# Performance work log

Measured on AMD Instinct MI355X. Metric: run time of the kernel, lower is better.

## Reference

```python
import jax, jax.numpy as jnp
import numpy as np

B, T, D = 4, 2048, 1024
F = 4 * D  # Config.RWKV_INTERMIDATE_SIZE * hidden_dim
LN_EPS = 1e-3  # keras LayerNormalization default epsilon


def layer_norm(x, g, b, eps=LN_EPS):
    mu = jnp.mean(x, axis=-1, keepdims=True)
    var = jnp.mean(jnp.square(x - mu), axis=-1, keepdims=True)
    return (x - mu) * jax.lax.rsqrt(var + eps) * g + b


def setup_inputs() -> dict:
    ks = jax.random.split(jax.random.key(0), 24)
    g = lambda k, shape: (jax.random.normal(k, shape, jnp.float32)
                          * np.sqrt(2.0 / sum(shape)))  # ~glorot
    return {
        "x": jax.random.normal(ks[0], (B, T, D), jnp.float32),
        "s_cm": jnp.zeros((B, D), jnp.float32),
        "s_tm": jnp.zeros((B, D), jnp.float32),
        "s_num": jnp.zeros((B, D), jnp.float32),
        "s_den": jnp.zeros((B, D), jnp.float32),
        "s_q": jnp.zeros((B, D), jnp.float32),
        "ln1_g": jnp.ones((D,), jnp.float32),
        "ln1_b": jnp.zeros((D,), jnp.float32),
        "ln2_g": jnp.ones((D,), jnp.float32),
        "ln2_b": jnp.zeros((D,), jnp.float32),
        "tm_mix_k": jax.random.uniform(ks[1], (D,), jnp.float32, 0.0, 2.0 / D),
        "tm_mix_v": jax.random.uniform(ks[2], (D,), jnp.float32, 0.0, 2.0 / D),
        "tm_mix_r": jax.random.uniform(ks[3], (D,), jnp.float32, 0.0, (2.0 / D) ** 0.5),
        "tm_kw": g(ks[4], (D, D)),
        "tm_vw": g(ks[5], (D, D)),
        "tm_rw": g(ks[6], (D, D)),
        "time_decay": jax.random.uniform(ks[7], (D,), jnp.float32, 0.0, 0.1),
        "time_first": jax.random.uniform(ks[8], (D,), jnp.float32, 0.0, 0.05),
        "out_w": g(ks[9], (D, D)),
        "cm_mix_k": jax.random.uniform(ks[10], (D,), jnp.float32, 0.0, 2.0 / D),
        "cm_mix_r": jax.random.uniform(ks[11], (D,), jnp.float32, 0.0, 2.0 / D),
        "cm_kw": g(ks[12], (D, F)),
        "cm_vw": g(ks[13], (F, D)),
        "cm_rw": g(ks[14], (D, D)),
    }


def _shift(h, s):
    # token shift: prepend last-token state, drop last timestep
    return jnp.concatenate([s[:, None, :], h[:, :-1, :]], axis=1)


def reference(x, s_cm, s_tm, s_num, s_den, s_q,
              ln1_g, ln1_b, ln2_g, ln2_b,
              tm_mix_k, tm_mix_v, tm_mix_r, tm_kw, tm_vw, tm_rw,
              time_decay, time_first, out_w,
              cm_mix_k, cm_mix_r, cm_kw, cm_vw, cm_rw):
    # ---- time mixing ----
    h = layer_norm(x, ln1_g, ln1_b)  # [B,T,D]
    hs = _shift(h, s_tm)
    xk = h * tm_mix_k + hs * (1.0 - tm_mix_k)
    xv = h * tm_mix_v + hs * (1.0 - tm_mix_v)
    xr = h * tm_mix_r + hs * (1.0 - tm_mix_r)
    k = xk @ tm_kw  # [B,T,D]
    v = xv @ tm_vw
    r = jax.nn.sigmoid(xr @ tm_rw)
    w = -jnp.exp(time_decay)  # [D]

    def step(carry, kv):
        num, den, q = carry
        kt, vt = kv  # [B,D]
        mo = jnp.maximum(q, kt + time_first)
        e1 = jnp.exp(q - mo)
        e2 = jnp.exp(kt + time_first - mo)
        out = (e1 * num + e2 * vt) / (e1 * den + e2)
        ms = jnp.maximum(q + w, kt)
        e1s = jnp.exp(q + w - ms)
        e2s = jnp.exp(kt - ms)
        return (e1s * num + e2s * vt, e1s * den + e2s, ms), out

    (num, den, q), wkv = jax.lax.scan(
        step, (s_num, s_den, s_q),
        (k.transpose(1, 0, 2), v.transpose(1, 0, 2)))
    wkv = wkv.transpose(1, 0, 2)  # [B,T,D]
    x = x + (r * wkv) @ out_w

    # ---- channel mixing ----
    h2 = layer_norm(x, ln2_g, ln2_b)
    hs2 = _shift(h2, s_cm)
    xk2 = h2 * cm_mix_k + hs2 * (1.0 - cm_mix_k)
    xr2 = h2 * cm_mix_r + hs2 * (1.0 - cm_mix_r)
    kv = jnp.square(jax.nn.relu(xk2 @ cm_kw)) @ cm_vw  # [B,T,F] -> [B,T,D]
    x = x + jax.nn.sigmoid(xr2 @ cm_rw) * kv

    # new state: (cm_inputs, tm_inputs, num, den, q)
    return x, h2[:, -1], h[:, -1], num, den, q
```

## Files before the change

### kernel.cpp

```cpp
#include <hip/hip_runtime.h>

typedef unsigned short ushort_t;
typedef __attribute__((ext_vector_type(8))) short short8;
typedef __attribute__((ext_vector_type(4))) float f32x4;

#define B_ 4
#define T_ 2048
#define D_ 1024
#define F_ 4096
#define M_ (B_*T_)
#define CH_ 64
#define NC_ (T_/CH_)

#define AS1 __attribute__((address_space(1)))
#define AS3 __attribute__((address_space(3)))

__device__ __forceinline__ ushort_t f2bf(float f) {
  union { float f; unsigned u; } a; a.f = f;
  unsigned r = a.u + 0x7FFFu + ((a.u >> 16) & 1u);
  return (ushort_t)(r >> 16);
}

__device__ __forceinline__ void gl_lds16(const void* g, void* l) {
  __builtin_amdgcn_global_load_lds((AS1 void*)(__UINTPTR_TYPE__)g,
                                   (AS3 void*)l, 16, 0, 0);
}

__global__ __launch_bounds__(256) void tconv(const float* __restrict__ W,
                                             ushort_t* __restrict__ Wt,
                                             int K, int N) {
  __shared__ float tile[32][33];
  int tx = threadIdx.x, ty = threadIdx.y;
  int n0 = blockIdx.x * 32, k0 = blockIdx.y * 32;
  #pragma unroll
  for (int i = 0; i < 32; i += 8)
    tile[ty + i][tx] = W[(size_t)(k0 + ty + i) * N + n0 + tx];
  __syncthreads();
  #pragma unroll
  for (int i = 0; i < 32; i += 8)
    Wt[(size_t)(n0 + ty + i) * K + k0 + tx] = f2bf(tile[tx][ty + i]);
}

__global__ __launch_bounds__(256) void ln_fwd(const float* __restrict__ x,
                                              const float* __restrict__ g,
                                              const float* __restrict__ bb,
                                              float* __restrict__ h,
                                              float* __restrict__ last) {
  int row = blockIdx.x;
  int tid = threadIdx.x;
  float4 v = ((const float4*)(x + (size_t)row * D_))[tid];
  float s1 = v.x + v.y + v.z + v.w;
  float s2 = v.x * v.x + v.y * v.y + v.z * v.z + v.w * v.w;
  #pragma unroll
  for (int o = 32; o > 0; o >>= 1) { s1 += __shfl_down(s1, o); s2 += __shfl_down(s2, o); }
  __shared__ float r1[4], r2[4];
  if ((tid & 63) == 0) { r1[tid >> 6] = s1; r2[tid >> 6] = s2; }
  __syncthreads();
  s1 = r1[0] + r1[1] + r1[2] + r1[3];
  s2 = r2[0] + r2[1] + r2[2] + r2[3];
  float mu = s1 * (1.0f / D_);
  float rs = rsqrtf(s2 * (1.0f / D_) - mu * mu + 1e-3f);
  float4 gv = ((const float4*)g)[tid];
  float4 bv = ((const float4*)bb)[tid];
  float4 o4;
  o4.x = (v.x - mu) * rs * gv.x + bv.x;
  o4.y = (v.y - mu) * rs * gv.y + bv.y;
  o4.z = (v.z - mu) * rs * gv.z + bv.z;
  o4.w = (v.w - mu) * rs * gv.w + bv.w;
  ((float4*)(h + (size_t)row * D_))[tid] = o4;
  if ((row & (T_ - 1)) == T_ - 1)
    ((float4*)(last + (size_t)(row >> 11) * D_))[tid] = o4;
}

#define MIX1(c, p, f) f2bf((c) * (f) + (p) * (1.0f - (f)))

__global__ __launch_bounds__(256) void mix_tm(const float* __restrict__ h,
                                              const float* __restrict__ st,
                                              const float* __restrict__ mk,
                                              const float* __restrict__ mv,
                                              const float* __restrict__ mr,
                                              ushort_t* __restrict__ xk,
                                              ushort_t* __restrict__ xv,
                                              ushort_t* __restrict__ xr) {
  size_t qi = (size_t)blockIdx.x * 256 + threadIdx.x;
  int dq = (int)(qi & 255);
  size_t td = qi >> 8;
  int t = (int)(td & (T_ - 1));
  int b = (int)(td >> 11);
  float4 hc = ((const float4*)h)[qi];
  float4 hp = (t == 0) ? ((const float4*)st)[b * 256 + dq] : ((const float4*)h)[qi - 256];
  float4 k4 = ((const float4*)mk)[dq];
  float4 v4 = ((const float4*)mv)[dq];
  float4 r4 = ((const float4*)mr)[dq];
  ushort4 ok, ov, orr;
  ok.x = MIX1(hc.x, hp.x, k4.x); ok.y = MIX1(hc.y, hp.y, k4.y);
  ok.z = MIX1(hc.z, hp.z, k4.z); ok.w = MIX1(hc.w, hp.w, k4.w);
  ov.x = MIX1(hc.x, hp.x, v4.x); ov.y = MIX1(hc.y, hp.y, v4.y);
  ov.z = MIX1(hc.z, hp.z, v4.z); ov.w = MIX1(hc.w, hp.w, v4.w);
  orr.x = MIX1(hc.x, hp.x, r4.x); orr.y = MIX1(hc.y, hp.y, r4.y);
  orr.z = MIX1(hc.z, hp.z, r4.z); orr.w = MIX1(hc.w, hp.w, r4.w);
  ((ushort4*)xk)[qi] = ok;
  ((ushort4*)xv)[qi] = ov;
  ((ushort4*)xr)[qi] = orr;
}

__global__ __launch_bounds__(256) void mix_cm(const float* __restrict__ h,
                                              const float* __restrict__ st,
                                              const float* __restrict__ mk,
                                              const float* __restrict__ mr,
                                              ushort_t* __restrict__ xk,
                                              ushort_t* __restrict__ xr) {
  size_t qi = (size_t)blockIdx.x * 256 + threadIdx.x;
  int dq = (int)(qi & 255);
  size_t td = qi >> 8;
  int t = (int)(td & (T_ - 1));
  int b = (int)(td >> 11);
  float4 hc = ((const float4*)h)[qi];
  float4 hp = (t == 0) ? ((const float4*)st)[b * 256 + dq] : ((const float4*)h)[qi - 256];
  float4 k4 = ((const float4*)mk)[dq];
  float4 r4 = ((const float4*)mr)[dq];
  ushort4 ok, orr;
  ok.x = MIX1(hc.x, hp.x, k4.x); ok.y = MIX1(hc.y, hp.y, k4.y);
  ok.z = MIX1(hc.z, hp.z, k4.z); ok.w = MIX1(hc.w, hp.w, k4.w);
  orr.x = MIX1(hc.x, hp.x, r4.x); orr.y = MIX1(hc.y, hp.y, r4.y);
  orr.z = MIX1(hc.z, hp.z, r4.z); orr.w = MIX1(hc.w, hp.w, r4.w);
  ((ushort4*)xk)[qi] = ok;
  ((ushort4*)xr)[qi] = orr;
}

__global__ __launch_bounds__(256) void wkv_part1(const float* __restrict__ k,
                                                 const float* __restrict__ v,
                                                 const float* __restrict__ tdec,
                                                 float* __restrict__ cn,
                                                 float* __restrict__ cd,
                                                 float* __restrict__ cq) {
  int idx = blockIdx.x * 256 + threadIdx.x;
  int d = idx & (D_ - 1);
  int b = (idx >> 10) & (B_ - 1);
  int c = idx >> 12;
  float w = -__expf(tdec[d]);
  const float* kp = k + ((size_t)b * T_ + c * CH_) * D_ + d;
  const float* vp = v + ((size_t)b * T_ + c * CH_) * D_ + d;
  float num = 0.0f, den = 0.0f, q = -1e30f;
  for (int t0 = 0; t0 < CH_; t0 += 8) {
    float kt[8], vt[8];
    #pragma unroll
    for (int i = 0; i < 8; ++i) {
      size_t off = (size_t)(t0 + i) * D_;
      kt[i] = kp[off]; vt[i] = vp[off];
    }
    #pragma unroll
    for (int i = 0; i < 8; ++i) {
      float kk = kt[i];
      float ms = fmaxf(q + w, kk);
      float e1 = __expf(q + w - ms), e2 = __expf(kk - ms);
      num = e1 * num + e2 * vt[i];
      den = e1 * den + e2;
      q = ms;
    }
  }
  cn[idx] = num; cd[idx] = den; cq[idx] = q;
}

__global__ __launch_bounds__(256) void wkv_part2(const float* __restrict__ cn,
                                                 const float* __restrict__ cd,
                                                 const float* __restrict__ cq,
                                                 const float* __restrict__ sn,
                                                 const float* __restrict__ sd,
                                                 const float* __restrict__ sq,
                                                 const float* __restrict__ tdec,
                                                 float* __restrict__ pn,
                                                 float* __restrict__ pd,
                                                 float* __restrict__ pq,
                                                 float* __restrict__ on,
                                                 float* __restrict__ od,
                                                 float* __restrict__ oq) {
  int idx = blockIdx.x * 256 + threadIdx.x;
  int d = idx & (D_ - 1);
  float w = -__expf(tdec[d]);
  float wL = w * (float)CH_;
  float num = sn[idx], den = sd[idx], q = sq[idx];
  #pragma unroll 4
  for (int c = 0; c < NC_; ++c) {
    int j = (c << 12) + idx;
    pn[j] = num; pd[j] = den; pq[j] = q;
    float m2 = cq[j];
    float qn = fmaxf(q + wL, m2);
    float e1 = __expf(q + wL - qn), e2 = __expf(m2 - qn);
    num = e1 * num + e2 * cn[j];
    den = e1 * den + e2 * cd[j];
    q = qn;
  }
  on[idx] = num; od[idx] = den; oq[idx] = q;
}

__global__ __launch_bounds__(256) void wkv_part3(const float* __restrict__ k,
                                                 const float* __restrict__ v,
                                                 const float* __restrict__ r,
                                                 const float* __restrict__ pn,
                                                 const float* __restrict__ pd,
                                                 const float* __restrict__ pq,
                                                 const float* __restrict__ tdec,
                                                 const float* __restrict__ tfirst,
                                                 ushort_t* __restrict__ rwkv) {
  int idx = blockIdx.x * 256 + threadIdx.x;
  int d = idx & (D_ - 1);
  int b = (idx >> 10) & (B_ - 1);
  int c = idx >> 12;
  float w = -__expf(tdec[d]);
  float tf = tfirst[d];
  float num = pn[idx], den = pd[idx], q = pq[idx];
  size_t base = ((size_t)b * T_ + c * CH_) * D_ + d;
  const float* kp = k + base;
  const float* vp = v + base;
  const float* rp = r + base;
  ushort_t* op = rwkv + base;
  for (int t0 = 0; t0 < CH_; t0 += 8) {
    float kt[8], vt[8], rt[8];
    #pragma unroll
    for (int i = 0; i < 8; ++i) {
      size_t off = (size_t)(t0 + i) * D_;
      kt[i] = kp[off]; vt[i] = vp[off]; rt[i] = rp[off];
    }
    #pragma unroll
    for (int i = 0; i < 8; ++i) {
      float kk = kt[i];
      float mo = fmaxf(q, kk + tf);
      float e1 = __expf(q - mo), e2 = __expf(kk + tf - mo);
      float o = (e1 * num + e2 * vt[i]) / (e1 * den + e2);
      op[(size_t)(t0 + i) * D_] = f2bf(rt[i] * o);
      float ms = fmaxf(q + w, kk);
      float e1s = __expf(q + w - ms), e2s = __expf(kk - ms);
      num = e1s * num + e2s * vt[i];
      den = e1s * den + e2s;
      q = ms;
    }
  }
}

template <int EPI>
__global__ __launch_bounds__(256)
void gemm128(const ushort_t* __restrict__ A, const ushort_t* __restrict__ Bt,
             int N, int K,
             float* __restrict__ Cf, ushort_t* __restrict__ Cb,
             const float* __restrict__ X, const float* __restrict__ X2,
             const float* __restrict__ Xb) {
  __shared__ alignas(16) ushort_t sA[128 * 64];
  __shared__ alignas(16) ushort_t sB[128 * 64];
  const int tid = threadIdx.x;
  const int m0 = blockIdx.x * 128, n0 = blockIdx.y * 128;
  const int lane = tid & 63, wave = tid >> 6;
  const int wm = (wave >> 1) * 64, wn = (wave & 1) * 64;
  const int lr = lane & 15;
  const int lk = (lane >> 4) * 8;

  const ushort_t* ga = A + (size_t)(m0 + (tid >> 3)) * K + (tid & 7) * 8;
  const ushort_t* gb = Bt + (size_t)(n0 + (tid >> 3)) * K + (tid & 7) * 8;
  ushort_t* la = sA + tid * 8;
  ushort_t* lb = sB + tid * 8;

  f32x4 acc[4][4] = {};

  const int ksteps = K >> 6;
  for (int kt = 0; kt < ksteps; ++kt) {
    const int kof = kt * 64;
    #pragma unroll
    for (int i = 0; i < 4; ++i) {
      gl_lds16(ga + (size_t)(i * 32) * K + kof, la + i * 2048);
      gl_lds16(gb + (size_t)(i * 32) * K + kof, lb + i * 2048);
    }
    __syncthreads();
    short8 af[2][4], bfr[2][4];
    #pragma unroll
    for (int s = 0; s < 2; ++s)
      #pragma unroll
      for (int i = 0; i < 4; ++i) {
        af[s][i]  = *(const short8*)&sA[(wm + i * 16 + lr) * 64 + s * 32 + lk];
        bfr[s][i] = *(const short8*)&sB[(wn + i * 16 + lr) * 64 + s * 32 + lk];
      }
    #pragma unroll
    for (int s = 0; s < 2; ++s)
      #pragma unroll
      for (int mi = 0; mi < 4; ++mi)
        #pragma unroll
        for (int ni = 0; ni < 4; ++ni)
          acc[mi][ni] = __builtin_amdgcn_mfma_f32_16x16x32_bf16(
              af[s][mi], bfr[s][ni], acc[mi][ni], 0, 0, 0);
    __syncthreads();
  }

  #pragma unroll
  for (int mi = 0; mi < 4; ++mi)
    #pragma unroll
    for (int ni = 0; ni < 4; ++ni)
      #pragma unroll
      for (int j = 0; j < 4; ++j) {
        int row = m0 + wm + mi * 16 + ((lane >> 4) << 2) + j;
        int col = n0 + wn + ni * 16 + lr;
        size_t idx = (size_t)row * N + col;
        float v = acc[mi][ni][j];
        if (EPI == 0) {
          Cf[idx] = v;
        } else if (EPI == 1) {
          Cf[idx] = 1.0f / (1.0f + __expf(-v));
        } else if (EPI == 2) {
          Cf[idx] = X[idx] + v;
        } else if (EPI == 4) {
          float s = 1.0f / (1.0f + __expf(-v));
          Cf[idx] = X2[idx] + s * (X[idx] + Xb[idx]);
        }
      }
}

template <int EPI>
__global__ __launch_bounds__(512, 2)
void gemm256(const ushort_t* __restrict__ A, const ushort_t* __restrict__ Bt,
             int N, int K, int ktn,
             float* __restrict__ Cf, float* __restrict__ Cf2,
             ushort_t* __restrict__ Cb) {
  __shared__ alignas(16) ushort_t sA[2][256 * 64];
  __shared__ alignas(16) ushort_t sB[2][256 * 64];
  const int tid = threadIdx.x;
  const int lane = tid & 63;
  const int wave = tid >> 6;
  const int wr = wave >> 2, wc = wave & 3;
  const int l15 = lane & 15;
  const int kb = (lane >> 4) << 4;
  const int m0 = blockIdx.x * 256, n0 = blockIdx.y * 256;
  const int kt0 = blockIdx.z * ktn;
  const ushort_t* gA = A + (size_t)m0 * K + (size_t)kt0 * 64;
  const ushort_t* gB = Bt + (size_t)n0 * K + (size_t)kt0 * 64;

  const int sr = tid >> 3;
  const int sc8 = (tid & 7) ^ (sr & 7);
  const int scb = (tid & 7) * 16;

  auto stage = [&](int dbuf, int kt, int h) {
    const ushort_t* g = (h < 2) ? gA : gB;
    ushort_t* sb = (h < 2) ? sA[dbuf] : sB[dbuf];
    int rbase = (h & 1) * 128;
    #pragma unroll
    for (int i = 0; i < 2; ++i) {
      int row = rbase + i * 64 + sr;
      gl_lds16(g + (size_t)row * K + (size_t)kt * 64 + sc8 * 8,
               (char*)sb + row * 128 + scb);
    }
  };

  auto ld = [&](const ushort_t* sbuf, int row, int s5) -> short8 {
    int cb = ((s5 << 6) + kb) ^ ((row & 7) << 4);
    return *(const short8*)((const char*)sbuf + row * 128 + cb);
  };

  f32x4 acc[8][4] = {};

  stage(0, 0, 0); stage(0, 0, 1); stage(0, 0, 2); stage(0, 0, 3);

  for (int t = 0; t < ktn; ++t) {
    const int cur = t & 1, nxt = cur ^ 1;
    const bool more = (t + 1 < ktn);
    if (more) { stage(nxt, t + 1, 0); stage(nxt, t + 1, 1); }
    if (more) asm volatile("s_waitcnt vmcnt(4)" ::: "memory");
    else      asm volatile("s_waitcnt vmcnt(0)" ::: "memory");
    __builtin_amdgcn_s_barrier();

    const ushort_t* curA = sA[cur];
    const ushort_t* curB = sB[cur];
    short8 bfr[4][2];

#define G256_MFMA16(MI0, A00, A01, A10, A11)                                  \
    __builtin_amdgcn_s_setprio(1);                                            \
    _Pragma("unroll")                                                         \
    for (int ni = 0; ni < 4; ++ni) {                                          \
      acc[MI0][ni] = __builtin_amdgcn_mfma_f32_16x16x32_bf16(                 \
          A00, bfr[ni][0], acc[MI0][ni], 0, 0, 0);                            \
      acc[MI0][ni] = __builtin_amdgcn_mfma_f32_16x16x32_bf16(                 \
          A01, bfr[ni][1], acc[MI0][ni], 0, 0, 0);                            \
      acc[MI0 + 1][ni] = __builtin_amdgcn_mfma_f32_16x16x32_bf16(             \
          A10, bfr[ni][0], acc[MI0 + 1][ni], 0, 0, 0);                        \
      acc[MI0 + 1][ni] = __builtin_amdgcn_mfma_f32_16x16x32_bf16(             \
          A11, bfr[ni][1], acc[MI0 + 1][ni], 0, 0, 0);                        \
    }                                                                         \
    __builtin_amdgcn_s_setprio(0);

#define G256_SYNC_IN()                                                        \
    asm volatile("" ::: "memory");                                            \
    __builtin_amdgcn_s_barrier();                                             \
    asm volatile("s_waitcnt lgkmcnt(0)" ::: "memory");                        \
    __builtin_amdgcn_sched_barrier(0);

#define G256_SYNC_OUT()                                                       \
    asm volatile("" ::: "memory");                                            \
    __builtin_amdgcn_s_barrier();

    {
      #pragma unroll
      for (int ni = 0; ni < 4; ++ni)
        #pragma unroll
        for (int s = 0; s < 2; ++s)
          bfr[ni][s] = ld(curB, wc * 64 + ni * 16 + l15, s);
      short8 a00 = ld(curA, wr * 128 + 0 * 16 + l15, 0);
      short8 a01 = ld(curA, wr * 128 + 0 * 16 + l15, 1);
      short8 a10 = ld(curA, wr * 128 + 1 * 16 + l15, 0);
      short8 a11 = ld(curA, wr * 128 + 1 * 16 + l15, 1);
      if (more) stage(nxt, t + 1, 2);
      G256_SYNC_IN();
      G256_MFMA16(0, a00, a01, a10, a11);
      G256_SYNC_OUT();
    }
    {
      short8 a00 = ld(curA, wr * 128 + 2 * 16 + l15, 0);
      short8 a01 = ld(curA, wr * 128 + 2 * 16 + l15, 1);
      short8 a10 = ld(curA, wr * 128 + 3 * 16 + l15, 0);
      short8 a11 = ld(curA, wr * 128 + 3 * 16 + l15, 1);
      if (more) stage(nxt, t + 1, 3);
      G256_SYNC_IN();
      G256_MFMA16(2, a00, a01, a10, a11);
      G256_SYNC_OUT();
    }
    {
      short8 a00 = ld(curA, wr * 128 + 4 * 16 + l15, 0);
      short8 a01 = ld(curA, wr * 128 + 4 * 16 + l15, 1);
      short8 a10 = ld(curA, wr * 128 + 5 * 16 + l15, 0);
      short8 a11 = ld(curA, wr * 128 + 5 * 16 + l15, 1);
      G256_SYNC_IN();
      G256_MFMA16(4, a00, a01, a10, a11);
      G256_SYNC_OUT();
    }
    {
      short8 a00 = ld(curA, wr * 128 + 6 * 16 + l15, 0);
      short8 a01 = ld(curA, wr * 128 + 6 * 16 + l15, 1);
      short8 a10 = ld(curA, wr * 128 + 7 * 16 + l15, 0);
      short8 a11 = ld(curA, wr * 128 + 7 * 16 + l15, 1);
      G256_SYNC_IN();
      G256_MFMA16(6, a00, a01, a10, a11);
      G256_SYNC_OUT();
    }
  }

  float* cfp = Cf;
  if (EPI == 0 && blockIdx.z) cfp = Cf2;
  #pragma unroll
  for (int mi = 0; mi < 8; ++mi)
    #pragma unroll
    for (int ni = 0; ni < 4; ++ni)
      #pragma unroll
      for (int j = 0; j < 4; ++j) {
        int row = m0 + wr * 128 + mi * 16 + ((lane >> 4) << 2) + j;
        int col = n0 + wc * 64 + ni * 16 + l15;
        size_t idx = (size_t)row * N + col;
        float v = acc[mi][ni][j];
        if (EPI == 0) {
          cfp[idx] = v;
        } else {
          float tt = v > 0.0f ? v : 0.0f;
          Cb[idx] = f2bf(tt * tt);
        }
      }
}

extern "C" void kernel_launch(void* const* d_in, const int* in_sizes, int n_in,
                              void* d_out, int out_size, void* d_ws, size_t ws_size,
                              hipStream_t stream) {
  const float* x      = (const float*)d_in[0];
  const float* s_cm   = (const float*)d_in[1];
  const float* s_tm   = (const float*)d_in[2];
  const float* s_num  = (const float*)d_in[3];
  const float* s_den  = (const float*)d_in[4];
  const float* s_q    = (const float*)d_in[5];
  const float* ln1_g  = (const float*)d_in[6];
  const float* ln1_b  = (const float*)d_in[7];
  const float* ln2_g  = (const float*)d_in[8];
  const float* ln2_b  = (const float*)d_in[9];
  const float* tmk    = (const float*)d_in[10];
  const float* tmv    = (const float*)d_in[11];
  const float* tmr    = (const float*)d_in[12];
  const float* tm_kw  = (const float*)d_in[13];
  const float* tm_vw  = (const float*)d_in[14];
  const float* tm_rw  = (const float*)d_in[15];
  const float* tdec   = (const float*)d_in[16];
  const float* tfirst = (const float*)d_in[17];
  const float* out_w  = (const float*)d_in[18];
  const float* cmk    = (const float*)d_in[19];
  const float* cmr    = (const float*)d_in[20];
  const float* cm_kw  = (const float*)d_in[21];
  const float* cm_vw  = (const float*)d_in[22];
  const float* cm_rw  = (const float*)d_in[23];

  float* out   = (float*)d_out;
  float* o_x   = out;
  float* o_h2l = out + (size_t)M_ * D_;
  float* o_hl  = o_h2l + B_ * D_;
  float* o_num = o_hl + B_ * D_;
  float* o_den = o_num + B_ * D_;
  float* o_q   = o_den + B_ * D_;

  char* W = (char*)d_ws;
  const size_t MB = 1024 * 1024;
  ushort_t* w_tmk = (ushort_t*)(W + 0 * MB);
  ushort_t* w_tmv = (ushort_t*)(W + 2 * MB);
  ushort_t* w_tmr = (ushort_t*)(W + 4 * MB);
  ushort_t* w_out = (ushort_t*)(W + 6 * MB);
  ushort_t* w_cmk = (ushort_t*)(W + 8 * MB);
  ushort_t* w_cmv = (ushort_t*)(W + 16 * MB);
  ushort_t* w_cmr = (ushort_t*)(W + 24 * MB);
  float*    hbuf  = (float*)(W + 26 * MB);
  ushort_t* xk    = (ushort_t*)(W + 58 * MB);
  ushort_t* xv    = (ushort_t*)(W + 74 * MB);
  ushort_t* xr    = (ushort_t*)(W + 90 * MB);
  float*    kbuf  = (float*)(W + 106 * MB);
  float*    vbuf  = (float*)(W + 138 * MB);
  float*    rbuf  = (float*)(W + 170 * MB);
  ushort_t* rwkv  = xr;
  ushort_t* xk2   = xk;
  ushort_t* xr2   = xv;
  ushort_t* kk    = (ushort_t*)kbuf;
  float*    kv_a  = rbuf;
  float*    kv_b  = hbuf;

  float* cn = (float*)(W + 26 * MB + 0 * 512 * 1024);
  float* cd = (float*)(W + 26 * MB + 1 * 512 * 1024);
  float* cq = (float*)(W + 26 * MB + 2 * 512 * 1024);
  float* pn = (float*)(W + 26 * MB + 3 * 512 * 1024);
  float* pd = (float*)(W + 26 * MB + 4 * 512 * 1024);
  float* pq = (float*)(W + 26 * MB + 5 * 512 * 1024);

  dim3 tb(32, 8);
  tconv<<<dim3(D_/32, D_/32), tb, 0, stream>>>(tm_kw, w_tmk, D_, D_);
  tconv<<<dim3(D_/32, D_/32), tb, 0, stream>>>(tm_vw, w_tmv, D_, D_);
  tconv<<<dim3(D_/32, D_/32), tb, 0, stream>>>(tm_rw, w_tmr, D_, D_);
  tconv<<<dim3(D_/32, D_/32), tb, 0, stream>>>(out_w, w_out, D_, D_);
  tconv<<<dim3(F_/32, D_/32), tb, 0, stream>>>(cm_kw, w_cmk, D_, F_);
  tconv<<<dim3(D_/32, F_/32), tb, 0, stream>>>(cm_vw, w_cmv, F_, D_);
  tconv<<<dim3(D_/32, D_/32), tb, 0, stream>>>(cm_rw, w_cmr, D_, D_);

  ln_fwd<<<M_, 256, 0, stream>>>(x, ln1_g, ln1_b, hbuf, o_hl);
  mix_tm<<<(M_ * D_ / 4) / 256, 256, 0, stream>>>(hbuf, s_tm, tmk, tmv, tmr, xk, xv, xr);
  gemm128<0><<<dim3(M_/128, D_/128), 256, 0, stream>>>(xk, w_tmk, D_, D_, kbuf, nullptr, nullptr, nullptr, nullptr);
  gemm128<0><<<dim3(M_/128, D_/128), 256, 0, stream>>>(xv, w_tmv, D_, D_, vbuf, nullptr, nullptr, nullptr, nullptr);
  gemm128<1><<<dim3(M_/128, D_/128), 256, 0, stream>>>(xr, w_tmr, D_, D_, rbuf, nullptr, nullptr, nullptr, nullptr);

  wkv_part1<<<(NC_ * B_ * D_) / 256, 256, 0, stream>>>(kbuf, vbuf, tdec, cn, cd, cq);
  wkv_part2<<<(B_ * D_) / 256, 256, 0, stream>>>(cn, cd, cq, s_num, s_den, s_q, tdec,
                                                 pn, pd, pq, o_num, o_den, o_q);
  wkv_part3<<<(NC_ * B_ * D_) / 256, 256, 0, stream>>>(kbuf, vbuf, rbuf, pn, pd, pq,
                                                       tdec, tfirst, rwkv);

  gemm128<2><<<dim3(M_/128, D_/128), 256, 0, stream>>>(rwkv, w_out, D_, D_, o_x, nullptr, x, nullptr, nullptr);

  ln_fwd<<<M_, 256, 0, stream>>>(o_x, ln2_g, ln2_b, hbuf, o_h2l);
  mix_cm<<<(M_ * D_ / 4) / 256, 256, 0, stream>>>(hbuf, s_cm, cmk, cmr, xk2, xr2);
  gemm256<1><<<dim3(M_/256, F_/256, 1), 512, 0, stream>>>(xk2, w_cmk, F_, D_, D_/64,
                                                          nullptr, nullptr, kk);
  gemm256<0><<<dim3(M_/256, D_/256, 2), 512, 0, stream>>>(kk, w_cmv, D_, F_, F_/128,
                                                          kv_a, kv_b, nullptr);
  gemm128<4><<<dim3(M_/128, D_/128), 256, 0, stream>>>(xr2, w_cmr, D_, D_, o_x, nullptr,
                                                       kv_a, o_x, kv_b);
}
```

Measured before the change: 450.0 us.

## Fuse layernorm with token-shift mixing and move all GEMMs to 256-tile kernel

Layernorm and token-shift mixing now run in one kernel that recomputes the previous row's layernorm, so the fp32 normalized buffer is never written and read back. The three time-mix projections become a single batched launch of the 256-tile GEMM, with the matrix index taken from blockIdx.z, assuming xk/xv/xr and their weights sit contiguously in memory. The output and cm_r projections also move to the 256-tile GEMM with fused epilogues, and the 128-tile GEMM is removed. The cost is doubled layernorm reduction work, and the small-N GEMMs now launch far fewer blocks (128 blocks per launch at N=1024), which may leave compute units idle.

Measured after the change: 462.4 us. 1.03x slower.

```diff
diff --git a/kernel.cpp b/kernel.cpp
--- a/kernel.cpp
+++ b/kernel.cpp
@@ -41,91 +41,85 @@
     Wt[(size_t)(n0 + ty + i) * K + k0 + tx] = f2bf(tile[tx][ty + i]);
 }
 
-__global__ __launch_bounds__(256) void ln_fwd(const float* __restrict__ x,
-                                              const float* __restrict__ g,
-                                              const float* __restrict__ bb,
-                                              float* __restrict__ h,
-                                              float* __restrict__ last) {
+#define MIX1(c, p, f) f2bf((c) * (f) + (p) * (1.0f - (f)))
+
+template <int NOUT>
+__global__ __launch_bounds__(256)
+void ln_mix(const float* __restrict__ xin, const float* __restrict__ st,
+            const float* __restrict__ g, const float* __restrict__ bb,
+            const float* __restrict__ mk, const float* __restrict__ mv,
+            const float* __restrict__ mr,
+            ushort_t* __restrict__ ok, ushort_t* __restrict__ ov,
+            ushort_t* __restrict__ orr, float* __restrict__ last) {
   int row = blockIdx.x;
+  int t = row & (T_ - 1);
+  int b = row >> 11;
   int tid = threadIdx.x;
-  float4 v = ((const float4*)(x + (size_t)row * D_))[tid];
-  float s1 = v.x + v.y + v.z + v.w;
-  float s2 = v.x * v.x + v.y * v.y + v.z * v.z + v.w * v.w;
+  const bool pln = (t != 0);
+  float4 vc = ((const float4*)(xin + (size_t)row * D_))[tid];
+  float4 vp = pln ? ((const float4*)(xin + (size_t)(row - 1) * D_))[tid]
+                  : ((const float4*)(st + (size_t)b * D_))[tid];
+  float s0 = vc.x + vc.y + vc.z + vc.w;
+  float s1 = vc.x * vc.x + vc.y * vc.y + vc.z * vc.z + vc.w * vc.w;
+  float s2 = vp.x + vp.y + vp.z + vp.w;
+  float s3 = vp.x * vp.x + vp.y * vp.y + vp.z * vp.z + vp.w * vp.w;
   #pragma unroll
-  for (int o = 32; o > 0; o >>= 1) { s1 += __shfl_down(s1, o); s2 += __shfl_down(s2, o); }
-  __shared__ float r1[4], r2[4];
-  if ((tid & 63) == 0) { r1[tid >> 6] = s1; r2[tid >> 6] = s2; }
+  for (int o = 32; o > 0; o >>= 1) {
+    s0 += __shfl_down(s0, o); s1 += __shfl_down(s1, o);
+    s2 += __shfl_down(s2, o); s3 += __shfl_down(s3, o);
+  }
+  __shared__ float red[4][4];
+  if ((tid & 63) == 0) {
+    int w = tid >> 6;
+    red[w][0] = s0; red[w][1] = s1; red[w][2] = s2; red[w][3] = s3;
+  }
   __syncthreads();
-  s1 = r1[0] + r1[1] + r1[2] + r1[3];
-  s2 = r2[0] + r2[1] + r2[2] + r2[3];
-  float mu = s1 * (1.0f / D_);
-  float rs = rsqrtf(s2 * (1.0f / D_) - mu * mu + 1e-3f);
+  float cs0 = red[0][0] + red[1][0] + red[2][0] + red[3][0];
+  float cs1 = red[0][1] + red[1][1] + red[2][1] + red[3][1];
+  float ps0 = red[0][2] + red[1][2] + red[2][2] + red[3][2];
+  float ps1 = red[0][3] + red[1][3] + red[2][3] + red[3][3];
+
+  float mu = cs0 * (1.0f / D_);
+  float rs = rsqrtf(cs1 * (1.0f / D_) - mu * mu + 1e-3f);
   float4 gv = ((const float4*)g)[tid];
   float4 bv = ((const float4*)bb)[tid];
-  float4 o4;
-  o4.x = (v.x - mu) * rs * gv.x + bv.x;
-  o4.y = (v.y - mu) * rs * gv.y + bv.y;
-  o4.z = (v.z - mu) * rs * gv.z + bv.z;
-  o4.w = (v.w - mu) * rs * gv.w + bv.w;
-  ((float4*)(h + (size_t)row * D_))[tid] = o4;
-  if ((row & (T_ - 1)) == T_ - 1)
-    ((float4*)(last + (size_t)(row >> 11) * D_))[tid] = o4;
-}
-
-#define MIX1(c, p, f) f2bf((c) * (f) + (p) * (1.0f - (f)))
-
-__global__ __launch_bounds__(256) void mix_tm(const float* __restrict__ h,
-                                              const float* __restrict__ st,
-                                              const float* __restrict__ mk,
-                                              const float* __restrict__ mv,
-                                              const float* __restrict__ mr,
-                                              ushort_t* __restrict__ xk,
-                                              ushort_t* __restrict__ xv,
-                                              ushort_t* __restrict__ xr) {
-  size_t qi = (size_t)blockIdx.x * 256 + threadIdx.x;
-  int dq = (int)(qi & 255);
-  size_t td = qi >> 8;
-  int t = (int)(td & (T_ - 1));
-  int b = (int)(td >> 11);
-  float4 hc = ((const float4*)h)[qi];
-  float4 hp = (t == 0) ? ((const float4*)st)[b * 256 + dq] : ((const float4*)h)[qi - 256];
-  float4 k4 = ((const float4*)mk)[dq];
-  float4 v4 = ((const float4*)mv)[dq];
-  float4 r4 = ((const float4*)mr)[dq];
-  ushort4 ok, ov, orr;
-  ok.x = MIX1(hc.x, hp.x, k4.x); ok.y = MIX1(hc.y, hp.y, k4.y);
-  ok.z = MIX1(hc.z, hp.z, k4.z); ok.w = MIX1(hc.w, hp.w, k4.w);
-  ov.x = MIX1(hc.x, hp.x, v4.x); ov.y = MIX1(hc.y, hp.y, v4.y);
-  ov.z = MIX1(hc.z, hp.z, v4.z); ov.w = MIX1(hc.w, hp.w, v4.w);
-  orr.x = MIX1(hc.x, hp.x, r4.x); orr.y = MIX1(hc.y, hp.y, r4.y);
-  orr.z = MIX1(hc.z, hp.z, r4.z); orr.w = MIX1(hc.w, hp.w, r4.w);
-  ((ushort4*)xk)[qi] = ok;
-  ((ushort4*)xv)[qi] = ov;
-  ((ushort4*)xr)[qi] = orr;
-}
-
-__global__ __launch_bounds__(256) void mix_cm(const float* __restrict__ h,
-                                              const float* __restrict__ st,
-                                              const float* __restrict__ mk,
-                                              const float* __restrict__ mr,
-                                              ushort_t* __restrict__ xk,
-                                              ushort_t* __restrict__ xr) {
-  size_t qi = (size_t)blockIdx.x * 256 + threadIdx.x;
-  int dq = (int)(qi & 255);
-  size_t td = qi >> 8;
-  int t = (int)(td & (T_ - 1));
-  int b = (int)(td >> 11);
-  float4 hc = ((const float4*)h)[qi];
-  float4 hp = (t == 0) ? ((const float4*)st)[b * 256 + dq] : ((const float4*)h)[qi - 256];
-  float4 k4 = ((const float4*)mk)[dq];
-  float4 r4 = ((const float4*)mr)[dq];
-  ushort4 ok, orr;
-  ok.x = MIX1(hc.x, hp.x, k4.x); ok.y = MIX1(hc.y, hp.y, k4.y);
-  ok.z = MIX1(hc.z, hp.z, k4.z); ok.w = MIX1(hc.w, hp.w, k4.w);
-  orr.x = MIX1(hc.x, hp.x, r4.x); orr.y = MIX1(hc.y, hp.y, r4.y);
-  orr.z = MIX1(hc.z, hp.z, r4.z); orr.w = MIX1(hc.w, hp.w, r4.w);
-  ((ushort4*)xk)[qi] = ok;
-  ((ushort4*)xr)[qi] = orr;
+  float hc[4], hp[4];
+  hc[0] = (vc.x - mu) * rs * gv.x + bv.x;
+  hc[1] = (vc.y - mu) * rs * gv.y + bv.y;
+  hc[2] = (vc.z - mu) * rs * gv.z + bv.z;
+  hc[3] = (vc.w - mu) * rs * gv.w + bv.w;
+  if (pln) {
+    float mup = ps0 * (1.0f / D_);
+    float rsp = rsqrtf(ps1 * (1.0f / D_) - mup * mup + 1e-3f);
+    hp[0] = (vp.x - mup) * rsp * gv.x + bv.x;
+    hp[1] = (vp.y - mup) * rsp * gv.y + bv.y;
+    hp[2] = (vp.z - mup) * rsp * gv.z + bv.z;
+    hp[3] = (vp.w - mup) * rsp * gv.w + bv.w;
+  } else {
+    hp[0] = vp.x; hp[1] = vp.y; hp[2] = vp.z; hp[3] = vp.w;
+  }
+
+  size_t qi = (size_t)row * 256 + tid;
+  float4 k4 = ((const float4*)mk)[tid];
+  float4 r4 = ((const float4*)mr)[tid];
+  ushort4 o4;
+  o4.x = MIX1(hc[0], hp[0], k4.x); o4.y = MIX1(hc[1], hp[1], k4.y);
+  o4.z = MIX1(hc[2], hp[2], k4.z); o4.w = MIX1(hc[3], hp[3], k4.w);
+  ((ushort4*)ok)[qi] = o4;
+  if (NOUT == 3) {
+    float4 v4 = ((const float4*)mv)[tid];
+    o4.x = MIX1(hc[0], hp[0], v4.x); o4.y = MIX1(hc[1], hp[1], v4.y);
+    o4.z = MIX1(hc[2], hp[2], v4.z); o4.w = MIX1(hc[3], hp[3], v4.w);
+    ((ushort4*)ov)[qi] = o4;
+  }
+  o4.x = MIX1(hc[0], hp[0], r4.x); o4.y = MIX1(hc[1], hp[1], r4.y);
+  o4.z = MIX1(hc[2], hp[2], r4.z); o4.w = MIX1(hc[3], hp[3], r4.w);
+  ((ushort4*)orr)[qi] = o4;
+
+  if (t == T_ - 1) {
+    float4 h4; h4.x = hc[0]; h4.y = hc[1]; h4.z = hc[2]; h4.w = hc[3];
+    ((float4*)(last + (size_t)b * D_))[tid] = h4;
+  }
 }
 
 __global__ __launch_bounds__(256) void wkv_part1(const float* __restrict__ k,
@@ -239,84 +233,12 @@
 }
 
 template <int EPI>
-__global__ __launch_bounds__(256)
-void gemm128(const ushort_t* __restrict__ A, const ushort_t* __restrict__ Bt,
-             int N, int K,
-             float* __restrict__ Cf, ushort_t* __restrict__ Cb,
-             const float* __restrict__ X, const float* __restrict__ X2,
-             const float* __restrict__ Xb) {
-  __shared__ alignas(16) ushort_t sA[128 * 64];
-  __shared__ alignas(16) ushort_t sB[128 * 64];
-  const int tid = threadIdx.x;
-  const int m0 = blockIdx.x * 128, n0 = blockIdx.y * 128;
-  const int lane = tid & 63, wave = tid >> 6;
-  const int wm = (wave >> 1) * 64, wn = (wave & 1) * 64;
-  const int lr = lane & 15;
-  const int lk = (lane >> 4) * 8;
-
-  const ushort_t* ga = A + (size_t)(m0 + (tid >> 3)) * K + (tid & 7) * 8;
-  const ushort_t* gb = Bt + (size_t)(n0 + (tid >> 3)) * K + (tid & 7) * 8;
-  ushort_t* la = sA + tid * 8;
-  ushort_t* lb = sB + tid * 8;
-
-  f32x4 acc[4][4] = {};
-
-  const int ksteps = K >> 6;
-  for (int kt = 0; kt < ksteps; ++kt) {
-    const int kof = kt * 64;
-    #pragma unroll
-    for (int i = 0; i < 4; ++i) {
-      gl_lds16(ga + (size_t)(i * 32) * K + kof, la + i * 2048);
-      gl_lds16(gb + (size_t)(i * 32) * K + kof, lb + i * 2048);
-    }
-    __syncthreads();
-    short8 af[2][4], bfr[2][4];
-    #pragma unroll
-    for (int s = 0; s < 2; ++s)
-      #pragma unroll
-      for (int i = 0; i < 4; ++i) {
-        af[s][i]  = *(const short8*)&sA[(wm + i * 16 + lr) * 64 + s * 32 + lk];
-        bfr[s][i] = *(const short8*)&sB[(wn + i * 16 + lr) * 64 + s * 32 + lk];
-      }
-    #pragma unroll
-    for (int s = 0; s < 2; ++s)
-      #pragma unroll
-      for (int mi = 0; mi < 4; ++mi)
-        #pragma unroll
-        for (int ni = 0; ni < 4; ++ni)
-          acc[mi][ni] = __builtin_amdgcn_mfma_f32_16x16x32_bf16(
-              af[s][mi], bfr[s][ni], acc[mi][ni], 0, 0, 0);
-    __syncthreads();
-  }
-
-  #pragma unroll
-  for (int mi = 0; mi < 4; ++mi)
-    #pragma unroll
-    for (int ni = 0; ni < 4; ++ni)
-      #pragma unroll
-      for (int j = 0; j < 4; ++j) {
-        int row = m0 + wm + mi * 16 + ((lane >> 4) << 2) + j;
-        int col = n0 + wn + ni * 16 + lr;
-        size_t idx = (size_t)row * N + col;
-        float v = acc[mi][ni][j];
-        if (EPI == 0) {
-          Cf[idx] = v;
-        } else if (EPI == 1) {
-          Cf[idx] = 1.0f / (1.0f + __expf(-v));
-        } else if (EPI == 2) {
-          Cf[idx] = X[idx] + v;
-        } else if (EPI == 4) {
-          float s = 1.0f / (1.0f + __expf(-v));
-          Cf[idx] = X2[idx] + s * (X[idx] + Xb[idx]);
-        }
-      }
-}
-
-template <int EPI>
 __global__ __launch_bounds__(512, 2)
 void gemm256(const ushort_t* __restrict__ A, const ushort_t* __restrict__ Bt,
              int N, int K, int ktn,
              float* __restrict__ Cf, float* __restrict__ Cf2,
+             float* __restrict__ Cf3,
+             const float* __restrict__ X, const float* __restrict__ X2,
              ushort_t* __restrict__ Cb) {
   __shared__ alignas(16) ushort_t sA[2][256 * 64];
   __shared__ alignas(16) ushort_t sB[2][256 * 64];
@@ -327,9 +249,19 @@
   const int l15 = lane & 15;
   const int kb = (lane >> 4) << 4;
   const int m0 = blockIdx.x * 256, n0 = blockIdx.y * 256;
-  const int kt0 = blockIdx.z * ktn;
-  const ushort_t* gA = A + (size_t)m0 * K + (size_t)kt0 * 64;
-  const ushort_t* gB = Bt + (size_t)n0 * K + (size_t)kt0 * 64;
+  const int zid = blockIdx.z;
+
+  const ushort_t* Ause = A;
+  const ushort_t* Buse = Bt;
+  int kt0 = 0;
+  if (EPI == 3) {
+    Ause = A + (size_t)zid * M_ * D_;
+    Buse = Bt + (size_t)zid * D_ * D_;
+  } else if (EPI == 0) {
+    kt0 = zid * ktn;
+  }
+  const ushort_t* gA = Ause + (size_t)m0 * K + (size_t)kt0 * 64;
+  const ushort_t* gB = Buse + (size_t)n0 * K + (size_t)kt0 * 64;
 
   const int sr = tid >> 3;
   const int sc8 = (tid & 7) ^ (sr & 7);
@@ -439,7 +371,8 @@
   }
 
   float* cfp = Cf;
-  if (EPI == 0 && blockIdx.z) cfp = Cf2;
+  if (EPI == 0 && zid) cfp = Cf2;
+  if (EPI == 3) cfp = (zid == 0) ? Cf : (zid == 1 ? Cf2 : Cf3);
   #pragma unroll
   for (int mi = 0; mi < 8; ++mi)
     #pragma unroll
@@ -452,9 +385,16 @@
         float v = acc[mi][ni][j];
         if (EPI == 0) {
           cfp[idx] = v;
-        } else {
+        } else if (EPI == 1) {
           float tt = v > 0.0f ? v : 0.0f;
           Cb[idx] = f2bf(tt * tt);
+        } else if (EPI == 2) {
+          cfp[idx] = X[idx] + v;
+        } else if (EPI == 3) {
+          cfp[idx] = (zid == 2) ? 1.0f / (1.0f + __expf(-v)) : v;
+        } else if (EPI == 4) {
+          float s = 1.0f / (1.0f + __expf(-v));
+          cfp[idx] = X2[idx] + s * (X[idx] + Cf3[idx]);
         }
       }
 }
@@ -534,11 +474,10 @@
   tconv<<<dim3(D_/32, F_/32), tb, 0, stream>>>(cm_vw, w_cmv, F_, D_);
   tconv<<<dim3(D_/32, D_/32), tb, 0, stream>>>(cm_rw, w_cmr, D_, D_);
 
-  ln_fwd<<<M_, 256, 0, stream>>>(x, ln1_g, ln1_b, hbuf, o_hl);
-  mix_tm<<<(M_ * D_ / 4) / 256, 256, 0, stream>>>(hbuf, s_tm, tmk, tmv, tmr, xk, xv, xr);
-  gemm128<0><<<dim3(M_/128, D_/128), 256, 0, stream>>>(xk, w_tmk, D_, D_, kbuf, nullptr, nullptr, nullptr, nullptr);
-  gemm128<0><<<dim3(M_/128, D_/128), 256, 0, stream>>>(xv, w_tmv, D_, D_, vbuf, nullptr, nullptr, nullptr, nullptr);
-  gemm128<1><<<dim3(M_/128, D_/128), 256, 0, stream>>>(xr, w_tmr, D_, D_, rbuf, nullptr, nullptr, nullptr, nullptr);
+  ln_mix<3><<<M_, 256, 0, stream>>>(x, s_tm, ln1_g, ln1_b, tmk, tmv, tmr,
+                                    xk, xv, xr, o_hl);
+  gemm256<3><<<dim3(M_/256, D_/256, 3), 512, 0, stream>>>(
+      xk, w_tmk, D_, D_, D_/64, kbuf, vbuf, rbuf, nullptr, nullptr, nullptr);
 
   wkv_part1<<<(NC_ * B_ * D_) / 256, 256, 0, stream>>>(kbuf, vbuf, tdec, cn, cd, cq);
   wkv_part2<<<(B_ * D_) / 256, 256, 0, stream>>>(cn, cd, cq, s_num, s_den, s_q, tdec,
@@ -546,14 +485,15 @@
   wkv_part3<<<(NC_ * B_ * D_) / 256, 256, 0, stream>>>(kbuf, vbuf, rbuf, pn, pd, pq,
                                                        tdec, tfirst, rwkv);
 
-  gemm128<2><<<dim3(M_/128, D_/128), 256, 0, stream>>>(rwkv, w_out, D_, D_, o_x, nullptr, x, nullptr, nullptr);
-
-  ln_fwd<<<M_, 256, 0, stream>>>(o_x, ln2_g, ln2_b, hbuf, o_h2l);
-  mix_cm<<<(M_ * D_ / 4) / 256, 256, 0, stream>>>(hbuf, s_cm, cmk, cmr, xk2, xr2);
-  gemm256<1><<<dim3(M_/256, F_/256, 1), 512, 0, stream>>>(xk2, w_cmk, F_, D_, D_/64,
-                                                          nullptr, nullptr, kk);
-  gemm256<0><<<dim3(M_/256, D_/256, 2), 512, 0, stream>>>(kk, w_cmv, D_, F_, F_/128,
-                                                          kv_a, kv_b, nullptr);
-  gemm128<4><<<dim3(M_/128, D_/128), 256, 0, stream>>>(xr2, w_cmr, D_, D_, o_x, nullptr,
-                                                       kv_a, o_x, kv_b);
-}
+  gemm256<2><<<dim3(M_/256, D_/256, 1), 512, 0, stream>>>(
+      rwkv, w_out, D_, D_, D_/64, o_x, nullptr, nullptr, x, nullptr, nullptr);
+
+  ln_mix<2><<<M_, 256, 0, stream>>>(o_x, s_cm, ln2_g, ln2_b, cmk, nullptr, cmr,
+                                    xk2, nullptr, xr2, o_h2l);
+  gemm256<1><<<dim3(M_/256, F_/256, 1), 512, 0, stream>>>(
+      xk2, w_cmk, F_, D_, D_/64, nullptr, nullptr, nullptr, nullptr, nullptr, kk);
+  gemm256<0><<<dim3(M_/256, D_/256, 2), 512, 0, stream>>>(
+      kk, w_cmv, D_, F_, F_/128, kv_a, kv_b, nullptr, nullptr, nullptr, nullptr);
+  gemm256<4><<<dim3(M_/256, D_/256, 1), 512, 0, stream>>>(
+      xr2, w_cmr, D_, D_, D_/64, o_x, nullptr, kv_b, kv_a, o_x, nullptr);
+}
```
